# Performance work log

Measured on AMD Instinct MI355X. Metric: run time of the kernel, lower is better.

The kernel has to match this reference:

```python
import jax, jax.numpy as jnp
import numpy as np
from jax import lax

# Hyperparameters from init_kwargs (inference/testing path of the RPN)
PRE_NMS = 6000        # pre_nms_top_n['testing']
POST_NMS = 1000       # post_nms_top_n['testing']
NMS_THRESH = 0.7
MIN_SIZE = 1.0
WX = WY = WW = WH = 1.0                      # reg_weights
BBOX_XFORM_CLIP = float(np.log(1000.0 / 16.0))  # standard BoxCoder clamp on dw/dh


def _decode(deltas, anchors):
    # deltas, anchors: [K, 4] -> decoded boxes [K, 4] (x1,y1,x2,y2)
    wa = anchors[:, 2] - anchors[:, 0]
    ha = anchors[:, 3] - anchors[:, 1]
    cxa = anchors[:, 0] + 0.5 * wa
    cya = anchors[:, 1] + 0.5 * ha
    dx = deltas[:, 0] / WX
    dy = deltas[:, 1] / WY
    dw = jnp.minimum(deltas[:, 2] / WW, BBOX_XFORM_CLIP)
    dh = jnp.minimum(deltas[:, 3] / WH, BBOX_XFORM_CLIP)
    cx = dx * wa + cxa
    cy = dy * ha + cya
    w = jnp.exp(dw) * wa
    h = jnp.exp(dh) * ha
    return jnp.stack([cx - 0.5 * w, cy - 0.5 * h, cx + 0.5 * w, cy + 0.5 * h], axis=-1)


def _nms_keep(boxes, valid, thresh):
    # Sequential NMS over score-sorted boxes [K,4]; 'valid' marks non-removed boxes.
    K = boxes.shape[0]
    x1, y1, x2, y2 = boxes[:, 0], boxes[:, 1], boxes[:, 2], boxes[:, 3]
    areas = (x2 - x1) * (y2 - y1)
    idxs = jnp.arange(K)

    def body(i, keep):
        xx1 = jnp.maximum(x1[i], x1)
        yy1 = jnp.maximum(y1[i], y1)
        xx2 = jnp.minimum(x2[i], x2)
        yy2 = jnp.minimum(y2[i], y2)
        inter = jnp.maximum(xx2 - xx1, 0.0) * jnp.maximum(yy2 - yy1, 0.0)
        iou = inter / (areas[i] + areas - inter + 1e-9)
        suppress = (iou > thresh) & (idxs > i)
        return jnp.where(keep[i], keep & ~suppress, keep)

    return lax.fori_loop(0, K, body, valid)


def _proposals_one(anchors, objectness, deltas, img_h, img_w):
    # anchors [N,4], objectness [N], deltas [N,4] -> proposals [POST_NMS, 4]
    k = min(objectness.shape[0], PRE_NMS)
    scores, idx = lax.top_k(objectness, k)          # topk filter (sorted desc)
    boxes = _decode(deltas[idx], anchors[idx])      # anchor decode on top-k only
    # process_box: clip to image, filter small boxes (masked, not removed, for jit)
    x1 = jnp.clip(boxes[:, 0], 0.0, img_w)
    y1 = jnp.clip(boxes[:, 1], 0.0, img_h)
    x2 = jnp.clip(boxes[:, 2], 0.0, img_w)
    y2 = jnp.clip(boxes[:, 3], 0.0, img_h)
    boxes = jnp.stack([x1, y1, x2, y2], axis=-1)
    valid = ((x2 - x1) >= MIN_SIZE) & ((y2 - y1) >= MIN_SIZE)
    keep = _nms_keep(boxes, valid, NMS_THRESH)
    # Compact kept boxes (score order) into a fixed [POST_NMS,4] buffer, zero-padded
    rank = jnp.cumsum(keep.astype(jnp.int32)) - 1
    tgt = jnp.where(keep & (rank < POST_NMS), rank, POST_NMS)  # POST_NMS -> dropped
    out = jnp.zeros((POST_NMS, 4), boxes.dtype).at[tgt].set(boxes, mode='drop')
    return out


def setup_inputs() -> dict:
    key = jax.random.key(0)
    k1, k2, k3, k4 = jax.random.split(key, 4)
    B, N = 8, 500000
    IMG = 1024
    # Valid anchor boxes: random centers in-image, sizes in [16, 256]
    cxy = jax.random.uniform(k1, (B, N, 2), jnp.float32, 0.0, float(IMG))
    wh = jax.random.uniform(k2, (B, N, 2), jnp.float32, 16.0, 256.0)
    anchors = jnp.concatenate([cxy - 0.5 * wh, cxy + 0.5 * wh], axis=-1)
    objectness = jax.random.normal(k3, (B, N), jnp.float32)
    pred_bbox_delta = 0.1 * jax.random.normal(k4, (B, N, 4), jnp.float32)
    return {"anchors": anchors, "objectness": objectness,
            "pred_bbox_delta": pred_bbox_delta, "img_h": IMG, "img_w": IMG}


def reference(anchors, objectness, pred_bbox_delta, img_h, img_w):
    h, w = float(img_h), float(img_w)
    f = jax.vmap(lambda a, o, d: _proposals_one(a, o, d, h, w))
    return f(anchors, objectness, pred_bbox_delta)  # [B, POST_NMS, 4]
```

## Files before the change

### kernel.cpp

```cpp
#include <hip/hip_runtime.h>
#include <cstdint>
#include <cmath>

#define NBATCH   8
#define NPB      500000
#define PRE_NMS  6000
#define POST_NMS 1000
#define NWORDS   94
#define NBINS    16384
#define CANDCAP  8192
#define BBOX_CLIP 4.135166556742356f
#define NMS_THR  0.7f
#define TI 8
#define TJ 512
#define WIN 16
#define CNT_PAD 64
#define SORT_CHUNK 2048

#define F_SORT 1u
#define F_COMP 2u
#define F_OOB  4u

__device__ __forceinline__ unsigned monot(float f) {
    unsigned b = __float_as_uint(f);
    return (b & 0x80000000u) ? ~b : (b | 0x80000000u);
}

__global__ __launch_bounds__(256) void hist_kernel(const float* __restrict__ obj,
                                                   unsigned* __restrict__ hist) {
    __shared__ unsigned lh[NBINS];
    const int b = blockIdx.y;
    for (int q = threadIdx.x; q < NBINS; q += 256) lh[q] = 0;
    __syncthreads();
    const float* p = obj + (size_t)b * NPB;
    const int stride = gridDim.x * 256;
    for (int i = blockIdx.x * 256 + threadIdx.x; i < NPB; i += stride) {
        unsigned u = monot(p[i]);
        atomicAdd(&lh[u >> 18], 1u);
    }
    __syncthreads();
    unsigned* gh = hist + (size_t)b * NBINS;
    for (int q = threadIdx.x; q < NBINS; q += 256) {
        unsigned v = lh[q];
        if (v) atomicAdd(&gh[q], v);
    }
}

__global__ __launch_bounds__(256) void thresh_kernel(const unsigned* __restrict__ hist,
                                                     unsigned* __restrict__ tbin) {
    __shared__ unsigned part[256], pre[256];
    const int b = blockIdx.x;
    const unsigned* gh = hist + (size_t)b * NBINS;
    const int t = threadIdx.x;
    const int PER = NBINS / 256;
    unsigned s = 0;
    for (int d = 0; d < PER; ++d) s += gh[NBINS - 1 - (t * PER + d)];
    part[t] = s;
    __syncthreads();
    if (t == 0) {
        unsigned run = 0;
        for (int q = 0; q < 256; ++q) { pre[q] = run; run += part[q]; }
    }
    __syncthreads();
    unsigned c = pre[t];
    if (c < PRE_NMS && c + part[t] >= PRE_NMS) {
        unsigned run = c;
        for (int d = 0; d < PER; ++d) {
            int bin = NBINS - 1 - (t * PER + d);
            run += gh[bin];
            if (run >= PRE_NMS) { tbin[b] = (unsigned)bin; break; }
        }
    }
}

__global__ __launch_bounds__(256) void compact_kernel(const float* __restrict__ obj,
                                                      const unsigned* __restrict__ tbin,
                                                      unsigned long long* __restrict__ cand,
                                                      unsigned* __restrict__ ccnt) {
    const int b = blockIdx.y;
    const unsigned T = tbin[b];
    const float* p = obj + (size_t)b * NPB;
    unsigned long long* cb = cand + (size_t)b * CANDCAP;
    const int lane = threadIdx.x & 63;
    const int stride = gridDim.x * 256;
    for (int i = blockIdx.x * 256 + threadIdx.x; i < NPB; i += stride) {
        unsigned u = monot(p[i]);
        const bool pred = (u >> 18) >= T;
        unsigned long long bal = __ballot(pred);
        if (bal == 0) continue;
        unsigned base = 0;
        if (lane == 0) base = atomicAdd(&ccnt[(size_t)b * CNT_PAD], __popcll(bal));
        base = (unsigned)__shfl((int)base, 0);
        if (pred) {
            unsigned pos = base + (unsigned)__popcll(bal & ((1ULL << lane) - 1ULL));
            if (pos < CANDCAP)
                cb[pos] = ((unsigned long long)u << 32) | (unsigned)(~i);
        }
    }
}

__global__ __launch_bounds__(512) void sort_local_kernel(unsigned long long* __restrict__ cand) {
    __shared__ unsigned long long s[SORT_CHUNK];
    const int blk = blockIdx.x;
    const int b = blk >> 2, c = blk & 3;
    unsigned long long* cb = cand + (size_t)b * CANDCAP + (size_t)c * SORT_CHUNK;
    const int t = threadIdx.x;
    for (int i = t; i < SORT_CHUNK; i += 512) s[i] = cb[i];
    __syncthreads();
    for (unsigned k = 2; k <= SORT_CHUNK; k <<= 1) {
        const bool kfull = (k == SORT_CHUNK);
        const bool upfull = (c & 1) == 0;
        for (unsigned j = k >> 1; j > 0; j >>= 1) {
            for (unsigned ii = t; ii < SORT_CHUNK; ii += 512) {
                unsigned l = ii ^ j;
                if (l > ii) {
                    unsigned long long a = s[ii], d = s[l];
                    bool up = kfull ? upfull : ((ii & k) == 0);
                    if (up ? (a < d) : (a > d)) { s[ii] = d; s[l] = a; }
                }
            }
            __syncthreads();
        }
    }
    for (int i = t; i < SORT_CHUNK; i += 512) cb[i] = s[i];
}

__global__ __launch_bounds__(1024) void sort_merge_kernel(const unsigned long long* __restrict__ cand,
                                                          const float* __restrict__ obj,
                                                          unsigned* __restrict__ topk,
                                                          unsigned* __restrict__ flags) {
    __shared__ unsigned long long s[CANDCAP];
    const int b = blockIdx.x, t = threadIdx.x;
    const unsigned long long* cb = cand + (size_t)b * CANDCAP;
    for (int i = t; i < CANDCAP; i += 1024) s[i] = cb[i];
    __syncthreads();
    for (unsigned k = 2 * SORT_CHUNK; k <= CANDCAP; k <<= 1) {
        for (unsigned j = k >> 1; j > 0; j >>= 1) {
            for (unsigned ii = t; ii < CANDCAP; ii += 1024) {
                unsigned l = ii ^ j;
                if (l > ii) {
                    unsigned long long a = s[ii], c = s[l];
                    bool up = (ii & k) == 0;
                    if (up ? (a < c) : (a > c)) { s[ii] = c; s[l] = a; }
                }
            }
            __syncthreads();
        }
    }
    unsigned f = 0;
    for (int r = t; r < PRE_NMS; r += 1024) {
        unsigned long long c = s[r];
        unsigned idx = ~(unsigned)(c & 0xffffffffULL);
        if (idx >= NPB) { f |= F_OOB; idx = 0; }
        else if (monot(obj[(size_t)b * NPB + idx]) != (unsigned)(c >> 32)) f |= F_COMP;
        if (r < PRE_NMS - 1 && !(c > s[r + 1])) f |= F_SORT;
        topk[(size_t)b * PRE_NMS + r] = idx;
    }
    if (f) atomicOr(&flags[b], f);
}

__global__ __launch_bounds__(256) void decode_kernel(const float* __restrict__ anchors,
                                                     const float* __restrict__ deltas,
                                                     const unsigned* __restrict__ topk,
                                                     const int* __restrict__ imh,
                                                     const int* __restrict__ imw,
                                                     float* __restrict__ boxes,
                                                     float* __restrict__ areas,
                                                     unsigned long long* __restrict__ validm) {
    const int b = blockIdx.y;
    const int r = blockIdx.x * 256 + threadIdx.x;
    const bool active = r < PRE_NMS;
    int vh = imh[0], vw = imw[0];
    float ih = (vh > 0 && vh < (1 << 20)) ? (float)vh : __int_as_float(vh);
    float iw = (vw > 0 && vw < (1 << 20)) ? (float)vw : __int_as_float(vw);
    bool valid = false;
    if (active) {
        unsigned idx = topk[(size_t)b * PRE_NMS + r];
        if (idx >= NPB) idx = 0;
        const float4 a = ((const float4*)anchors)[(size_t)b * NPB + idx];
        const float4 d = ((const float4*)deltas)[(size_t)b * NPB + idx];
        float wa = a.z - a.x, ha = a.w - a.y;
        float cxa = a.x + 0.5f * wa, cya = a.y + 0.5f * ha;
        float dw = fminf(d.z, BBOX_CLIP), dh = fminf(d.w, BBOX_CLIP);
        float cx = __fadd_rn(__fmul_rn(d.x, wa), cxa);
        float cy = __fadd_rn(__fmul_rn(d.y, ha), cya);
        float ew = (float)::exp((double)dw), eh = (float)::exp((double)dh);
        float w = __fmul_rn(ew, wa), h = __fmul_rn(eh, ha);
        float x1 = cx - 0.5f * w, y1 = cy - 0.5f * h;
        float x2 = cx + 0.5f * w, y2 = cy + 0.5f * h;
        x1 = fminf(fmaxf(x1, 0.f), iw); y1 = fminf(fmaxf(y1, 0.f), ih);
        x2 = fminf(fmaxf(x2, 0.f), iw); y2 = fminf(fmaxf(y2, 0.f), ih);
        valid = (x2 - x1 >= 1.0f) && (y2 - y1 >= 1.0f);
        ((float4*)boxes)[(size_t)b * PRE_NMS + r] = make_float4(x1, y1, x2, y2);
        areas[(size_t)b * PRE_NMS + r] = __fmul_rn(x2 - x1, y2 - y1);
    }
    unsigned long long bal = __ballot(valid);
    int w = r >> 6;
    if ((threadIdx.x & 63) == 0 && w < NWORDS) validm[(size_t)b * NWORDS + w] = bal;
}

__global__ __launch_bounds__(256) void mask_kernel(const float* __restrict__ boxes,
                                                   const float* __restrict__ areas,
                                                   unsigned long long* __restrict__ mask) {
    __shared__ float4 sb[TJ];
    __shared__ float  sa[TJ];
    const int b = blockIdx.x & 7;
    const int i0 = (blockIdx.x >> 3) * TI;
    const int jbase = (i0 >> 6) << 6;
    const int wv = threadIdx.x >> 6, ln = threadIdx.x & 63;
    const int ia = i0 + 2 * wv, ic = ia + 1;
    const float4 bA = ((const float4*)boxes)[(size_t)b * PRE_NMS + ia];
    const float4 bC = ((const float4*)boxes)[(size_t)b * PRE_NMS + ic];
    const float aA = areas[(size_t)b * PRE_NMS + ia];
    const float aC = areas[(size_t)b * PRE_NMS + ic];
    unsigned long long* rowA = mask + ((size_t)b * PRE_NMS + ia) * NWORDS;
    unsigned long long* rowC = mask + ((size_t)b * PRE_NMS + ic) * NWORDS;
    const int wA = ia >> 6, wC = ic >> 6;
    for (int t0 = jbase; t0 < NWORDS * 64; t0 += TJ) {
        for (int e = threadIdx.x; e < TJ; e += 256) {
            int j = t0 + e;
            if (j < PRE_NMS) {
                sb[e] = ((const float4*)boxes)[(size_t)b * PRE_NMS + j];
                sa[e] = areas[(size_t)b * PRE_NMS + j];
            } else { sb[e] = make_float4(0.f, 0.f, 0.f, 0.f); sa[e] = 0.f; }
        }
        __syncthreads();
        for (int wl = 0; wl < TJ / 64; ++wl) {
            const int w = (t0 >> 6) + wl;
            if (w >= NWORDS) break;
            const int e = wl * 64 + ln;
            const int j = t0 + e;
            const float4 bj = sb[e];
            const float aj = sa[e];
            bool pA = false, pC = false;
            if (j < PRE_NMS) {
                float xx1 = fmaxf(bA.x, bj.x), yy1 = fmaxf(bA.y, bj.y);
                float xx2 = fminf(bA.z, bj.z), yy2 = fminf(bA.w, bj.w);
                float inter = __fmul_rn(fmaxf(__fsub_rn(xx2, xx1), 0.f),
                                        fmaxf(__fsub_rn(yy2, yy1), 0.f));
                float den = __fadd_rn(__fsub_rn(__fadd_rn(aA, aj), inter), 1e-9f);
                pA = (j > ia) && (__fdiv_rn(inter, den) > NMS_THR);
                xx1 = fmaxf(bC.x, bj.x); yy1 = fmaxf(bC.y, bj.y);
                xx2 = fminf(bC.z, bj.z); yy2 = fminf(bC.w, bj.w);
                inter = __fmul_rn(fmaxf(__fsub_rn(xx2, xx1), 0.f),
                                  fmaxf(__fsub_rn(yy2, yy1), 0.f));
                den = __fadd_rn(__fsub_rn(__fadd_rn(aC, aj), inter), 1e-9f);
                pC = (j > ic) && (__fdiv_rn(inter, den) > NMS_THR);
            }
            unsigned long long mA = __ballot(pA), mC = __ballot(pC);
            if (ln == 0) {
                if (w >= wA) rowA[w] = mA;
                if (w >= wC) rowC[w] = mC;
            }
        }
        __syncthreads();
    }
}

__global__ __launch_bounds__(64) void scan_kernel(const unsigned long long* __restrict__ mask,
                                                  const unsigned long long* __restrict__ validm,
                                                  const float* __restrict__ boxes,
                                                  const unsigned* __restrict__ flags,
                                                  const unsigned* __restrict__ ccnt,
                                                  float* __restrict__ out) {
    const int b = blockIdx.x, lane = threadIdx.x;
    const unsigned long long* mb = mask + (size_t)b * PRE_NMS * NWORDS;
    const int w0 = 2 * lane, w1 = 2 * lane + 1;
    unsigned long long r_lo = (w0 < NWORDS) ? ~validm[(size_t)b * NWORDS + w0] : ~0ULL;
    unsigned long long r_hi = (w1 < NWORDS) ? ~validm[(size_t)b * NWORDS + w1] : ~0ULL;
    int count = 0;

    uint4 MA[WIN], MB[WIN], MC[WIN];
    unsigned long long WA[WIN], WB[WIN], WC[WIN];
    float4 bxA, bxB, bxC;

#define ISSUE(M, W, BX, base_)                                                   \
    {                                                                            \
        const int bb_ = (base_);                                                 \
        const char* rb_ = (const char*)(mb + (size_t)bb_ * NWORDS);              \
        const int wI_ = bb_ >> 6;                                                \
        _Pragma("unroll")                                                        \
        for (int q = 0; q < WIN; ++q) {                                          \
            const char* rp_ = rb_ + (size_t)q * (NWORDS * 8);                    \
            M[q] = *(const uint4*)(rp_ + (size_t)lane * 16);                     \
            W[q] = *(const unsigned long long*)(rp_ + (size_t)wI_ * 8);          \
        }                                                                        \
        BX = (lane < WIN)                                                        \
                 ? ((const float4*)boxes)[(size_t)b * PRE_NMS + bb_ + lane]      \
                 : make_float4(0.f, 0.f, 0.f, 0.f);                              \
    }

#define RESOLVE(M, W, BX, base_)                                                 \
    {                                                                            \
        const int bb_ = (base_);                                                 \
        const int wR_ = bb_ >> 6, s0_ = bb_ & 63;                                \
        const unsigned long long sel_ = (wR_ & 1) ? r_hi : r_lo;                 \
        const int srcl_ = wR_ >> 1;                                              \
        const unsigned lo_ = (unsigned)__shfl((int)(unsigned)(sel_ & 0xffffffffULL), srcl_); \
        const unsigned hi_ = (unsigned)__shfl((int)(unsigned)(sel_ >> 32), srcl_);           \
        const unsigned long long ww_ = ((unsigned long long)hi_ << 32) | lo_;    \
        unsigned cand_ = (unsigned)((~ww_) >> s0_) & 0xFFFFu;                    \
        unsigned kept_ = 0;                                                      \
        const int cb_ = count;                                                   \
        _Pragma("unroll")                                                        \
        for (int q = 0; q < WIN; ++q) {                                          \
            if (((cand_ >> q) & 1u) && count < POST_NMS) {                       \
                kept_ |= 1u << q; ++count;                                       \
                cand_ &= ~(unsigned)(W[q] >> s0_);                               \
            }                                                                    \
        }                                                                        \
        const bool v0_ = (w0 >= wR_), v1_ = (w1 >= wR_);                         \
        _Pragma("unroll")                                                        \
        for (int q = 0; q < WIN; ++q) {                                          \
            if (kept_ & (1u << q)) {                                             \
                const uint4 m_ = M[q];                                           \
                if (v0_) r_lo |= ((unsigned long long)m_.y << 32) | m_.x;        \
                if (v1_) r_hi |= ((unsigned long long)m_.w << 32) | m_.z;        \
            }                                                                    \
        }                                                                        \
        if (lane < WIN && (kept_ & (1u << lane))) {                              \
            const int rank_ = cb_ + __popc(kept_ & ((1u << lane) - 1u));         \
            ((float4*)out)[(size_t)b * POST_NMS + rank_] = BX;                   \
        }                                                                        \
    }

    ISSUE(MA, WA, bxA, 0)
    ISSUE(MB, WB, bxB, WIN)
    bool done = false;
    for (int base = 0; base < PRE_NMS && !done; base += 3 * WIN) {
        const int n2 = base + 2 * WIN;
        ISSUE(MC, WC, bxC, (n2 < PRE_NMS) ? n2 : 0)
        RESOLVE(MA, WA, bxA, base)
        done = (count >= POST_NMS);
        if (!done) {
            const int n3 = base + 3 * WIN;
            ISSUE(MA, WA, bxA, (n3 < PRE_NMS) ? n3 : 0)
            RESOLVE(MB, WB, bxB, base + WIN)
            done = (count >= POST_NMS);
        }
        if (!done) {
            const int n4 = base + 4 * WIN;
            ISSUE(MB, WB, bxB, (n4 < PRE_NMS) ? n4 : 0)
            RESOLVE(MC, WC, bxC, base + 2 * WIN)
            done = (count >= POST_NMS);
        }
    }
#undef ISSUE
#undef RESOLVE

    if (lane == 0) {
        float canary = 0.f;
        const unsigned cc = ccnt[(size_t)b * CNT_PAD];
        const unsigned fl = flags[b];
        if (cc > CANDCAP)       canary = 111000.f;
        else if (cc < PRE_NMS)  canary = 222000.f;
        if (fl & F_SORT)        canary = 333000.f;
        if (fl & F_COMP)        canary = 444000.f;
        if (fl & F_OOB)         canary = 777000.f;
        if (canary != 0.f) out[(size_t)b * POST_NMS * 4] = canary;
    }
}

extern "C" void kernel_launch(void* const* d_in, const int* in_sizes, int n_in,
                              void* d_out, int out_size, void* d_ws, size_t ws_size,
                              hipStream_t stream) {
    const float* anchors = (const float*)d_in[0];
    const float* obj     = (const float*)d_in[1];
    const float* deltas  = (const float*)d_in[2];
    const int*   imh     = (const int*)d_in[3];
    const int*   imw     = (const int*)d_in[4];
    float* out = (float*)d_out;
    char* ws = (char*)d_ws;

    size_t off = 0;
    auto alloc = [&](size_t bytes) {
        size_t o = off;
        off = (off + bytes + 511) & ~(size_t)511;
        return o;
    };
    const size_t HIST  = alloc((size_t)NBATCH * NBINS * 4);
    const size_t TBIN  = alloc((size_t)NBATCH * 4);
    const size_t CCNT  = alloc((size_t)NBATCH * CNT_PAD * 4);
    const size_t FLAGS = alloc((size_t)NBATCH * 4);
    const size_t CAND  = alloc((size_t)NBATCH * CANDCAP * 8);
    const size_t ZEND  = off;
    const size_t TOPK  = alloc((size_t)NBATCH * PRE_NMS * 4);
    const size_t BOX   = alloc((size_t)NBATCH * PRE_NMS * 16);
    const size_t AREA  = alloc((size_t)NBATCH * PRE_NMS * 4);
    const size_t VALID = alloc((size_t)NBATCH * NWORDS * 8);
    const size_t MASK  = alloc((size_t)NBATCH * PRE_NMS * NWORDS * 8);
    (void)alloc(1024);
    if (ws_size < off) return;

    unsigned*            hist   = (unsigned*)(ws + HIST);
    unsigned*            tbin   = (unsigned*)(ws + TBIN);
    unsigned*            ccnt   = (unsigned*)(ws + CCNT);
    unsigned*            flags  = (unsigned*)(ws + FLAGS);
    unsigned long long*  cand   = (unsigned long long*)(ws + CAND);
    unsigned*            topk   = (unsigned*)(ws + TOPK);
    float*               boxes  = (float*)(ws + BOX);
    float*               areas  = (float*)(ws + AREA);
    unsigned long long*  validm = (unsigned long long*)(ws + VALID);
    unsigned long long*  maskp  = (unsigned long long*)(ws + MASK);

    hipMemsetAsync(ws, 0, ZEND, stream);
    hipMemsetAsync(out, 0, (size_t)out_size * sizeof(float), stream);

    hist_kernel      <<<dim3(32, NBATCH), 256, 0, stream>>>(obj, hist);
    thresh_kernel    <<<dim3(NBATCH), 256, 0, stream>>>(hist, tbin);
    compact_kernel   <<<dim3(128, NBATCH), 256, 0, stream>>>(obj, tbin, cand, ccnt);
    sort_local_kernel<<<dim3(NBATCH * (CANDCAP / SORT_CHUNK)), 512, 0, stream>>>(cand);
    sort_merge_kernel<<<dim3(NBATCH), 1024, 0, stream>>>(cand, obj, topk, flags);
    decode_kernel    <<<dim3((PRE_NMS + 255) / 256, NBATCH), 256, 0, stream>>>(
        anchors, deltas, topk, imh, imw, boxes, areas, validm);
    mask_kernel      <<<dim3((PRE_NMS / TI) * NBATCH), 256, 0, stream>>>(boxes, areas, maskp);
    scan_kernel      <<<dim3(NBATCH), 64, 0, stream>>>(maskp, validm, boxes, flags, ccnt, out);
    (void)in_sizes; (void)n_in; (void)ws_size;
}
```

Measured before the change: 405.9 us.

## Process four rows per wavefront in NMS mask kernel and drop the division

The IoU mask kernel now gives each wavefront four query boxes instead of two, which doubles the rows per block (TI 8→16). Each shared-memory column tile is therefore reused across more rows and half as many blocks reload it. The correctly rounded float division plus compare is replaced by a double-precision multiply compare against the midpoint between 0.7f and the next float, meant to reproduce the rounded-division result without a divide. The risks are higher register pressure and fewer blocks, which may lower occupancy, and slower FP64 if that path is costly.

New measurement: 379.2 us. -6.6%, faster.

```diff
diff --git a/kernel.cpp b/kernel.cpp
--- a/kernel.cpp
+++ b/kernel.cpp
@@ -10,8 +10,7 @@
 #define NBINS    16384
 #define CANDCAP  8192
 #define BBOX_CLIP 4.135166556742356f
-#define NMS_THR  0.7f
-#define TI 8
+#define TI 16
 #define TJ 512
 #define WIN 16
 #define CNT_PAD 64
@@ -24,6 +23,11 @@
 __device__ __forceinline__ unsigned monot(float f) {
     unsigned b = __float_as_uint(f);
     return (b & 0x80000000u) ? ~b : (b | 0x80000000u);
+}
+
+__device__ __forceinline__ bool iou_gt_thr(float inter, float den) {
+    const double MID = (double)0.7f + 0x1p-25;
+    return (double)inter >= MID * (double)den;
 }
 
 __global__ __launch_bounds__(256) void hist_kernel(const float* __restrict__ obj,
@@ -208,14 +212,17 @@
     const int i0 = (blockIdx.x >> 3) * TI;
     const int jbase = (i0 >> 6) << 6;
     const int wv = threadIdx.x >> 6, ln = threadIdx.x & 63;
-    const int ia = i0 + 2 * wv, ic = ia + 1;
-    const float4 bA = ((const float4*)boxes)[(size_t)b * PRE_NMS + ia];
-    const float4 bC = ((const float4*)boxes)[(size_t)b * PRE_NMS + ic];
-    const float aA = areas[(size_t)b * PRE_NMS + ia];
-    const float aC = areas[(size_t)b * PRE_NMS + ic];
-    unsigned long long* rowA = mask + ((size_t)b * PRE_NMS + ia) * NWORDS;
-    unsigned long long* rowC = mask + ((size_t)b * PRE_NMS + ic) * NWORDS;
-    const int wA = ia >> 6, wC = ic >> 6;
+    const int ir = i0 + 4 * wv;
+    float4 bx[4]; float ar[4]; int wlo[4];
+    unsigned long long* rowp[4];
+#pragma unroll
+    for (int r = 0; r < 4; ++r) {
+        const int i = ir + r;
+        bx[r]   = ((const float4*)boxes)[(size_t)b * PRE_NMS + i];
+        ar[r]   = areas[(size_t)b * PRE_NMS + i];
+        rowp[r] = mask + ((size_t)b * PRE_NMS + i) * NWORDS;
+        wlo[r]  = i >> 6;
+    }
     for (int t0 = jbase; t0 < NWORDS * 64; t0 += TJ) {
         for (int e = threadIdx.x; e < TJ; e += 256) {
             int j = t0 + e;
@@ -232,25 +239,17 @@
             const int j = t0 + e;
             const float4 bj = sb[e];
             const float aj = sa[e];
-            bool pA = false, pC = false;
-            if (j < PRE_NMS) {
-                float xx1 = fmaxf(bA.x, bj.x), yy1 = fmaxf(bA.y, bj.y);
-                float xx2 = fminf(bA.z, bj.z), yy2 = fminf(bA.w, bj.w);
+            const bool jin = (j < PRE_NMS);
+#pragma unroll
+            for (int r = 0; r < 4; ++r) {
+                float xx1 = fmaxf(bx[r].x, bj.x), yy1 = fmaxf(bx[r].y, bj.y);
+                float xx2 = fminf(bx[r].z, bj.z), yy2 = fminf(bx[r].w, bj.w);
                 float inter = __fmul_rn(fmaxf(__fsub_rn(xx2, xx1), 0.f),
                                         fmaxf(__fsub_rn(yy2, yy1), 0.f));
-                float den = __fadd_rn(__fsub_rn(__fadd_rn(aA, aj), inter), 1e-9f);
-                pA = (j > ia) && (__fdiv_rn(inter, den) > NMS_THR);
-                xx1 = fmaxf(bC.x, bj.x); yy1 = fmaxf(bC.y, bj.y);
-                xx2 = fminf(bC.z, bj.z); yy2 = fminf(bC.w, bj.w);
-                inter = __fmul_rn(fmaxf(__fsub_rn(xx2, xx1), 0.f),
-                                  fmaxf(__fsub_rn(yy2, yy1), 0.f));
-                den = __fadd_rn(__fsub_rn(__fadd_rn(aC, aj), inter), 1e-9f);
-                pC = (j > ic) && (__fdiv_rn(inter, den) > NMS_THR);
-            }
-            unsigned long long mA = __ballot(pA), mC = __ballot(pC);
-            if (ln == 0) {
-                if (w >= wA) rowA[w] = mA;
-                if (w >= wC) rowC[w] = mC;
+                float den = __fadd_rn(__fsub_rn(__fadd_rn(ar[r], aj), inter), 1e-9f);
+                bool p = jin && (j > ir + r) && iou_gt_thr(inter, den);
+                unsigned long long m = __ballot(p);
+                if (ln == 0 && w >= wlo[r]) rowp[r][w] = m;
             }
         }
         __syncthreads();
```
